# Performance work log

Hardware: AMD Instinct MI355X
Metric: run time of the kernel (lower is better)

## Reference

```python
import jax, jax.numpy as jnp
import numpy as np

B, S, D_IN, D = 2, 192, 1024, 128  # batch, seq_len, input_dim, triaffine_dim


def setup_inputs() -> dict:
    key = jax.random.key(0)
    ks = jax.random.split(key, 10)
    g = lambda k, sh, sc: jax.random.normal(k, sh, jnp.float32) * sc
    return {
        "x": g(ks[0], (B, S, D_IN), 1.0),
        "Wp": g(ks[1], (D_IN, D), 0.02), "bp": jnp.zeros((D,), jnp.float32),
        "Wh": g(ks[2], (D_IN, D), 0.02), "bh": jnp.zeros((D,), jnp.float32),
        "Wt": g(ks[3], (D_IN, D), 0.02), "bt": jnp.zeros((D,), jnp.float32),
        "W_span_ph": g(ks[4], (D, D, D), 0.02),
        "W_span_pt": g(ks[5], (D, D, D), 0.02),
        "W_ph_sib": g(ks[6], (D, D, D), 0.02),
        "W_pt_sib": g(ks[7], (D, D, D), 0.02),
        "W_ph_cop": g(ks[8], (D, D, D), 0.02),
        "W_pt_cop": g(ks[9], (D, D, D), 0.02),
    }


def _mlp(x, W, b):
    # supar-style MLP: Linear + LeakyReLU(0.1); dropout is identity at eval time
    return jax.nn.leaky_relu(x @ W + b, negative_slope=0.1)


def _triaffine(x, y, z, w):
    # supar Triaffine (n_out=1, no bias): s[b,z,x,y] = x_i W_ikj z_k y_j
    wz = jnp.einsum('bzk,ikj->bzij', z, w)          # [b,s,d,d]
    return jnp.einsum('bxi,bzij,byj->bzxy', x, wz, y)  # [b,s,s,s]


def _sym(s):
    # s.triu() + s.triu(1).transpose(-1,-2) over last two dims
    n = s.shape[-1]
    up = jnp.triu(jnp.ones((n, n), bool))
    up1 = jnp.triu(jnp.ones((n, n), bool), 1)
    zero = jnp.zeros((), s.dtype)
    return jnp.where(up, s, zero) + jnp.swapaxes(jnp.where(up1, s, zero), -1, -2)


def reference(x, Wp, bp, Wh, bh, Wt, bt,
              W_span_ph, W_span_pt, W_ph_sib, W_pt_sib, W_ph_cop, W_pt_cop):
    p = _mlp(x, Wp, bp)
    sh = _mlp(x, Wh, bh)   # shared_span: sh_mlp = h_mlp
    st = _mlp(x, Wt, bt)   # shared_span: st_mlp = t_mlp
    span_pst = _sym(_triaffine(sh, st, p, W_span_pt))
    span_psh = _sym(_triaffine(sh, st, p, W_span_ph))
    ph_sib = _sym(_triaffine(sh, sh, p, W_ph_sib))
    pt_sib = _sym(_triaffine(st, st, p, W_pt_sib))
    # co-parent scores: [b,z,x,y] -> permute(0,2,3,1) -> [b,x,y,z]
    ph_cop = jnp.transpose(_triaffine(p, p, sh, W_ph_cop), (0, 2, 3, 1))
    pt_cop = jnp.transpose(_sym(_triaffine(p, p, st, W_pt_cop)), (0, 2, 3, 1))
    return (span_psh, span_pst, ph_sib, pt_sib, ph_cop, pt_cop)
```

## Files before the change

### kernel.cpp

```cpp
#include <hip/hip_runtime.h>

#define SS 192
#define DD 128
#define SAN 16384
#define PITCH 136

typedef short bf8v __attribute__((ext_vector_type(8)));
typedef float f4v  __attribute__((ext_vector_type(4)));

__device__ __forceinline__ unsigned short f2bf(float f) {
    union { float f; unsigned u; } v; v.f = f;
    unsigned r = v.u + 0x7fffu + ((v.u >> 16) & 1u);
    return (unsigned short)(r >> 16);
}

__device__ __forceinline__ f4v mfma16(bf8v a, bf8v b, f4v c) {
    return __builtin_amdgcn_mfma_f32_16x16x32_bf16(a, b, c, 0, 0, 0);
}

__global__ __launch_bounds__(256) void proj_part(
    const float* __restrict__ x,
    const float* __restrict__ Wp, const float* __restrict__ Wh,
    const float* __restrict__ Wt, float* __restrict__ part)
{
    __shared__ float xs[8 * 256];
    int r0 = blockIdx.x * 8;
    int w  = blockIdx.y;
    int kc = blockIdx.z;
    const float* W = (w == 0) ? Wp : (w == 1) ? Wh : Wt;
    int tid = threadIdx.x;
    for (int u = tid; u < 512; u += 256) {
        int row = u >> 6, k4 = u & 63;
        *(float4*)(&xs[row * 256 + k4 * 4]) =
            *(const float4*)(&x[(size_t)(r0 + row) * 1024 + kc * 256 + k4 * 4]);
    }
    __syncthreads();
    int col = tid & 127, rg = tid >> 7;
    float acc[4] = {0.f, 0.f, 0.f, 0.f};
    const float* Wk = W + (size_t)(kc * 256) * 128 + col;
    #pragma unroll 8
    for (int k = 0; k < 256; ++k) {
        float wv = Wk[(size_t)k * 128];
        #pragma unroll
        for (int r = 0; r < 4; ++r) acc[r] += xs[(rg * 4 + r) * 256 + k] * wv;
    }
    float* pp = part + (((size_t)w * 4 + kc) * 384) * 128;
    #pragma unroll
    for (int r = 0; r < 4; ++r)
        pp[(size_t)(r0 + rg * 4 + r) * 128 + col] = acc[r];
}

__global__ __launch_bounds__(256) void proj_fin(
    const float* __restrict__ part,
    const float* __restrict__ bp, const float* __restrict__ bh,
    const float* __restrict__ bt,
    unsigned short* __restrict__ Pb, unsigned short* __restrict__ SHb,
    unsigned short* __restrict__ STb)
{
    int r0 = blockIdx.x * 8;
    int w  = blockIdx.y;
    const float* bias = (w == 0) ? bp : (w == 1) ? bh : bt;
    unsigned short* O = (w == 0) ? Pb : (w == 1) ? SHb : STb;
    int tid = threadIdx.x;
    int col = tid & 127, rg = tid >> 7;
    const float* pw = part + ((size_t)w * 4) * 384 * 128;
    float bb = bias[col];
    #pragma unroll
    for (int r = 0; r < 4; ++r) {
        int row = r0 + rg * 4 + r;
        float s = pw[(size_t)row * 128 + col]
                + pw[(size_t)(384 + row) * 128 + col]
                + pw[(size_t)(2 * 384 + row) * 128 + col]
                + pw[(size_t)(3 * 384 + row) * 128 + col];
        s += bb;
        s = s > 0.f ? s : 0.1f * s;
        O[(size_t)row * 128 + col] = f2bf(s);
    }
}

__global__ __launch_bounds__(256) void prep_rev(
    const float* __restrict__ w0, const float* __restrict__ w1,
    const float* __restrict__ w2, const float* __restrict__ w3,
    unsigned short* __restrict__ Wprep)
{
    __shared__ float tile[32][33];
    int sel = blockIdx.z;
    const float* in = (sel == 0) ? w0 : (sel == 1) ? w1 : (sel == 2) ? w2 : w3;
    unsigned short* out = Wprep + (size_t)sel * 2097152;
    int i  = blockIdx.y;
    int kt = (blockIdx.x >> 2) * 32, jt = (blockIdx.x & 3) * 32;
    int tx = threadIdx.x & 31, ty = threadIdx.x >> 5;
    #pragma unroll
    for (int r = 0; r < 4; ++r) {
        int k = kt + ty + r * 8;
        tile[ty + r * 8][tx] = in[((size_t)i * 128 + k) * 128 + jt + tx];
    }
    __syncthreads();
    #pragma unroll
    for (int r = 0; r < 4; ++r) {
        int j = jt + ty + r * 8;
        out[((size_t)j * 128 + i) * 128 + kt + tx] = f2bf(tile[tx][ty + r * 8]);
    }
}

__global__ __launch_bounds__(256) void prep_cop(
    const float* __restrict__ in0, const float* __restrict__ in1,
    unsigned short* __restrict__ Wprep)
{
    __shared__ float tile[32][33];
    int sel = blockIdx.z;
    const float* in = sel ? in1 : in0;
    unsigned short* out = Wprep + (size_t)(4 + sel) * 2097152;
    int k  = blockIdx.y;
    int it = (blockIdx.x >> 2) * 32, jt = (blockIdx.x & 3) * 32;
    int tx = threadIdx.x & 31, ty = threadIdx.x >> 5;
    #pragma unroll
    for (int r = 0; r < 4; ++r) {
        int i = it + ty + r * 8;
        tile[ty + r * 8][tx] = in[((size_t)i * 128 + k) * 128 + jt + tx];
    }
    __syncthreads();
    #pragma unroll
    for (int r = 0; r < 4; ++r) {
        int j = jt + ty + r * 8;
        out[((size_t)j * 128 + k) * 128 + it + tx] = f2bf(tile[tx][ty + r * 8]);
    }
}

__global__ __launch_bounds__(256) void stageA(
    const unsigned short* __restrict__ Pb,
    const unsigned short* __restrict__ Wprep, unsigned short* __restrict__ SAout)
{
    __shared__ unsigned short BL[64 * PITCH];
    int slot = blockIdx.y;
    int n0 = blockIdx.x * 64;
    const unsigned short* Wn = Wprep + (size_t)slot * 2097152 + (size_t)n0 * 128;
    unsigned short* Oo = SAout + (size_t)slot * ((size_t)384 * SAN);
    int tid = threadIdx.x;
    for (int u = tid; u < 1024; u += 256) {
        int e = u * 8; int r = e >> 7; int c = e & 127;
        *(uint4*)(&BL[r * PITCH + c]) = *(const uint4*)(&Wn[e]);
    }
    __syncthreads();
    int wave = tid >> 6, lane = tid & 63, m = lane & 15, quad = lane >> 4;
    const unsigned short* br = &BL[(wave * 16 + m) * PITCH + quad * 8];
    bf8v b0 = *(const bf8v*)(br);
    bf8v b1 = *(const bf8v*)(br + 32);
    bf8v b2 = *(const bf8v*)(br + 64);
    bf8v b3 = *(const bf8v*)(br + 96);
    for (int mt = 0; mt < 24; mt += 2) {
        const unsigned short* ar0 = Pb + (size_t)(mt * 16 + m) * 128 + quad * 8;
        const unsigned short* ar1 = ar0 + 16 * 128;
        f4v acc0 = {0.f, 0.f, 0.f, 0.f}, acc1 = {0.f, 0.f, 0.f, 0.f};
        acc0 = mfma16(*(const bf8v*)(ar0),      b0, acc0);
        acc1 = mfma16(*(const bf8v*)(ar1),      b0, acc1);
        acc0 = mfma16(*(const bf8v*)(ar0 + 32), b1, acc0);
        acc1 = mfma16(*(const bf8v*)(ar1 + 32), b1, acc1);
        acc0 = mfma16(*(const bf8v*)(ar0 + 64), b2, acc0);
        acc1 = mfma16(*(const bf8v*)(ar1 + 64), b2, acc1);
        acc0 = mfma16(*(const bf8v*)(ar0 + 96), b3, acc0);
        acc1 = mfma16(*(const bf8v*)(ar1 + 96), b3, acc1);
        unsigned short* orow0 = Oo + (size_t)(mt * 16) * SAN + n0 + wave * 16;
        unsigned short* orow1 = orow0 + (size_t)16 * SAN;
        #pragma unroll
        for (int r = 0; r < 4; ++r) {
            orow0[(size_t)(quad * 4 + r) * SAN + m] = f2bf(acc0[r]);
            orow1[(size_t)(quad * 4 + r) * SAN + m] = f2bf(acc1[r]);
        }
    }
}

__global__ __launch_bounds__(256, 3) void stageB_all(
    const unsigned short* __restrict__ Pb, const unsigned short* __restrict__ SHb,
    const unsigned short* __restrict__ STb, const unsigned short* __restrict__ SA,
    float* __restrict__ out)
{
    __shared__ unsigned short WZT[128 * PITCH];
    __shared__ unsigned short Tst[64 * PITCH];
    const size_t OUTN = (size_t)2 * SS * SS * SS;

    int t  = blockIdx.y;
    int bz = blockIdx.x;
    int b  = bz / SS;
    int tid = threadIdx.x;

    const unsigned short* src = SA + ((size_t)t * 384 + bz) * SAN;
    for (int u = tid; u < 2048; u += 256) {
        int e = u * 8; int j = e >> 7; int i = e & 127;
        *(uint4*)(&WZT[j * PITCH + i]) = *(const uint4*)(&src[e]);
    }
    __syncthreads();

    int wave = tid >> 6, lane = tid & 63, m = lane & 15, quad = lane >> 4;
    unsigned short* Trow = &Tst[wave * 16 * PITCH];
    const unsigned short* Ta = &Tst[(wave * 16 + m) * PITCH + quad * 8];

    if (t < 4) {
        const unsigned short* X = (t == 3) ? STb : SHb;
        const unsigned short* Y = (t == 2) ? SHb : STb;
        float* O = out + (size_t)t * OUTN + (size_t)bz * SS * SS;
        const unsigned short* Xb = X + (size_t)b * SS * DD;
        const unsigned short* Yb = Y + (size_t)b * SS * DD;

        int mts[3];
        mts[0] = wave;
        mts[1] = 7 - wave;
        mts[2] = (wave < 2) ? 9 - wave : 8 + wave;

        bf8v ta[3][4];
        #pragma unroll
        for (int mi = 0; mi < 3; ++mi) {
            int mt = mts[mi];
            const unsigned short* xr = Xb + (size_t)(mt * 16 + m) * DD + quad * 8;
            bf8v a0 = *(const bf8v*)(xr);
            bf8v a1 = *(const bf8v*)(xr + 32);
            bf8v a2 = *(const bf8v*)(xr + 64);
            bf8v a3 = *(const bf8v*)(xr + 96);
            for (int nt = 0; nt < 8; nt += 2) {
                f4v acc0 = {0.f,0.f,0.f,0.f}, acc1 = {0.f,0.f,0.f,0.f};
                const unsigned short* w0 = &WZT[(nt * 16 + m) * PITCH + quad * 8];
                const unsigned short* w1 = &WZT[((nt + 1) * 16 + m) * PITCH + quad * 8];
                acc0 = mfma16(a0, *(const bf8v*)(w0),      acc0);
                acc1 = mfma16(a0, *(const bf8v*)(w1),      acc1);
                acc0 = mfma16(a1, *(const bf8v*)(w0 + 32), acc0);
                acc1 = mfma16(a1, *(const bf8v*)(w1 + 32), acc1);
                acc0 = mfma16(a2, *(const bf8v*)(w0 + 64), acc0);
                acc1 = mfma16(a2, *(const bf8v*)(w1 + 64), acc1);
                acc0 = mfma16(a3, *(const bf8v*)(w0 + 96), acc0);
                acc1 = mfma16(a3, *(const bf8v*)(w1 + 96), acc1);
                #pragma unroll
                for (int r = 0; r < 4; ++r) {
                    Trow[(quad * 4 + r) * PITCH + nt * 16 + m]       = f2bf(acc0[r]);
                    Trow[(quad * 4 + r) * PITCH + (nt + 1) * 16 + m] = f2bf(acc1[r]);
                }
            }
            ta[mi][0] = *(const bf8v*)(Ta);
            ta[mi][1] = *(const bf8v*)(Ta + 32);
            ta[mi][2] = *(const bf8v*)(Ta + 64);
            ta[mi][3] = *(const bf8v*)(Ta + 96);
        }

        for (int yt = mts[0]; yt < 12; ++yt) {
            const unsigned short* yr = Yb + (size_t)(yt * 16 + m) * DD + quad * 8;
            bf8v yv0 = *(const bf8v*)(yr);
            bf8v yv1 = *(const bf8v*)(yr + 32);
            bf8v yv2 = *(const bf8v*)(yr + 64);
            bf8v yv3 = *(const bf8v*)(yr + 96);
            f4v accs[3];
            #pragma unroll
            for (int mi = 0; mi < 3; ++mi) {
                f4v acc = {0.f,0.f,0.f,0.f};
                acc = mfma16(ta[mi][0], yv0, acc);
                acc = mfma16(ta[mi][1], yv1, acc);
                acc = mfma16(ta[mi][2], yv2, acc);
                acc = mfma16(ta[mi][3], yv3, acc);
                accs[mi] = acc;
            }
            #pragma unroll
            for (int mi = 0; mi < 3; ++mi) {
                int mt = mts[mi];
                if (mt > yt) continue;
                f4v acc = accs[mi];
                int xs_ = mt * 16, ys_ = yt * 16, cc = m;
                if (mt == yt) {
                    #pragma unroll
                    for (int r = 0; r < 4; ++r) {
                        int rr = quad * 4 + r;
                        if (rr <= cc) O[(size_t)(xs_ + rr) * SS + xs_ + cc] = acc[r];
                        if (cc > rr)  O[(size_t)(xs_ + cc) * SS + xs_ + rr] = acc[r];
                    }
                } else {
                    #pragma unroll
                    for (int r = 0; r < 4; ++r)
                        O[(size_t)(xs_ + quad * 4 + r) * SS + ys_ + cc] = acc[r];
                    *(f4v*)(&O[(size_t)(ys_ + cc) * SS + xs_ + quad * 4]) = acc;
                }
            }
        }
    } else {
        const unsigned short* Zsrc = (t == 4) ? SHb : STb;
        int x  = bz - b * SS;
        int xt = x >> 4;
        float* Od = out + (size_t)t * OUTN + (size_t)bz * SS * SS;
        float* Om = out + (size_t)t * OUTN + (size_t)b * SS * SS * SS;

        bf8v tb[3][4];
        #pragma unroll
        for (int zi = 0; zi < 3; ++zi) {
            int zt = wave * 3 + zi;
            const unsigned short* sr = Zsrc + (size_t)(b * SS + zt * 16 + m) * DD + quad * 8;
            bf8v a0 = *(const bf8v*)(sr);
            bf8v a1 = *(const bf8v*)(sr + 32);
            bf8v a2 = *(const bf8v*)(sr + 64);
            bf8v a3 = *(const bf8v*)(sr + 96);
            for (int jt = 0; jt < 8; jt += 2) {
                f4v acc0 = {0.f,0.f,0.f,0.f}, acc1 = {0.f,0.f,0.f,0.f};
                const unsigned short* w0 = &WZT[(jt * 16 + m) * PITCH + quad * 8];
                const unsigned short* w1 = &WZT[((jt + 1) * 16 + m) * PITCH + quad * 8];
                acc0 = mfma16(a0, *(const bf8v*)(w0),      acc0);
                acc1 = mfma16(a0, *(const bf8v*)(w1),      acc1);
                acc0 = mfma16(a1, *(const bf8v*)(w0 + 32), acc0);
                acc1 = mfma16(a1, *(const bf8v*)(w1 + 32), acc1);
                acc0 = mfma16(a2, *(const bf8v*)(w0 + 64), acc0);
                acc1 = mfma16(a2, *(const bf8v*)(w1 + 64), acc1);
                acc0 = mfma16(a3, *(const bf8v*)(w0 + 96), acc0);
                acc1 = mfma16(a3, *(const bf8v*)(w1 + 96), acc1);
                #pragma unroll
                for (int r = 0; r < 4; ++r) {
                    Trow[(quad * 4 + r) * PITCH + jt * 16 + m]       = f2bf(acc0[r]);
                    Trow[(quad * 4 + r) * PITCH + (jt + 1) * 16 + m] = f2bf(acc1[r]);
                }
            }
            tb[zi][0] = *(const bf8v*)(Ta);
            tb[zi][1] = *(const bf8v*)(Ta + 32);
            tb[zi][2] = *(const bf8v*)(Ta + 64);
            tb[zi][3] = *(const bf8v*)(Ta + 96);
        }

        const unsigned short* Pbase = Pb + (size_t)b * SS * DD;
        int yt0 = (t == 4) ? 0 : xt;
        for (int yt = yt0; yt < 12; ++yt) {
            const unsigned short* pr = Pbase + (size_t)(yt * 16 + m) * DD + quad * 8;
            bf8v pv0 = *(const bf8v*)(pr);
            bf8v pv1 = *(const bf8v*)(pr + 32);
            bf8v pv2 = *(const bf8v*)(pr + 64);
            bf8v pv3 = *(const bf8v*)(pr + 96);
            f4v accs[3];
            #pragma unroll
            for (int zi = 0; zi < 3; ++zi) {
                f4v acc = {0.f,0.f,0.f,0.f};
                acc = mfma16(pv0, tb[zi][0], acc);
                acc = mfma16(pv1, tb[zi][1], acc);
                acc = mfma16(pv2, tb[zi][2], acc);
                acc = mfma16(pv3, tb[zi][3], acc);
                accs[zi] = acc;
            }
            if (t == 4) {
                #pragma unroll
                for (int zi = 0; zi < 3; ++zi) {
                    int zc = (wave * 3 + zi) * 16 + m;
                    #pragma unroll
                    for (int r = 0; r < 4; ++r)
                        Od[(size_t)(yt * 16 + quad * 4 + r) * SS + zc] = accs[zi][r];
                }
            } else if (yt == xt) {
                #pragma unroll
                for (int zi = 0; zi < 3; ++zi) {
                    int zc = (wave * 3 + zi) * 16 + m;
                    #pragma unroll
                    for (int r = 0; r < 4; ++r) {
                        int y = yt * 16 + quad * 4 + r;
                        if (y >= x) Od[(size_t)y * SS + zc] = accs[zi][r];
                        if (y > x)  Om[(size_t)y * SS * SS + (size_t)x * SS + zc] = accs[zi][r];
                    }
                }
            } else {
                #pragma unroll
                for (int zi = 0; zi < 3; ++zi) {
                    int zc = (wave * 3 + zi) * 16 + m;
                    #pragma unroll
                    for (int r = 0; r < 4; ++r) {
                        int y = yt * 16 + quad * 4 + r;
                        Od[(size_t)y * SS + zc] = accs[zi][r];
                        Om[(size_t)y * SS * SS + (size_t)x * SS + zc] = accs[zi][r];
                    }
                }
            }
        }
    }
}

extern "C" void kernel_launch(void* const* d_in, const int* in_sizes, int n_in,
                              void* d_out, int out_size, void* d_ws, size_t ws_size,
                              hipStream_t stream)
{
    const float* x   = (const float*)d_in[0];
    const float* Wp  = (const float*)d_in[1];
    const float* bp  = (const float*)d_in[2];
    const float* Wh  = (const float*)d_in[3];
    const float* bh  = (const float*)d_in[4];
    const float* Wt  = (const float*)d_in[5];
    const float* bt  = (const float*)d_in[6];
    const float* W_span_ph = (const float*)d_in[7];
    const float* W_span_pt = (const float*)d_in[8];
    const float* W_ph_sib  = (const float*)d_in[9];
    const float* W_pt_sib  = (const float*)d_in[10];
    const float* W_ph_cop  = (const float*)d_in[11];
    const float* W_pt_cop  = (const float*)d_in[12];

    char* ws = (char*)d_ws;
    unsigned short* Pb    = (unsigned short*)ws;
    unsigned short* SHb   = Pb + 384 * 128;
    unsigned short* STb   = SHb + 384 * 128;
    unsigned short* Wprep = (unsigned short*)(ws + 294912);
    unsigned short* SA    = (unsigned short*)(ws + 294912 + (size_t)6 * 2097152 * 2);
    float* part = (float*)SA;

    float* out  = (float*)d_out;

    proj_part<<<dim3(48, 3, 4), 256, 0, stream>>>(x, Wp, Wh, Wt, part);
    proj_fin<<<dim3(48, 3), 256, 0, stream>>>(part, bp, bh, bt, Pb, SHb, STb);
    prep_rev<<<dim3(16, 128, 4), 256, 0, stream>>>(W_span_ph, W_span_pt, W_ph_sib,
                                                   W_pt_sib, Wprep);
    prep_cop<<<dim3(16, 128, 2), 256, 0, stream>>>(W_ph_cop, W_pt_cop, Wprep);
    stageA<<<dim3(256, 6), 256, 0, stream>>>(Pb, Wprep, SA);
    stageB_all<<<dim3(384, 6), 256, 0, stream>>>(Pb, SHb, STb, SA, out);
}
```

Before: 563.6 us.

## Double stageB block to 8 waves, rebalance tiles, pack bf16 LDS stores, merge prep kernels

StageB now launches 512 threads (8 waves) per block instead of 4, and each wave handles one or two 16-row tiles instead of three. The symmetric span paths pair tiles wave and 15-wave so the triangular work stays balanced. Phase-1 results are computed with swapped MFMA operands so each lane writes packed bf16 pairs to LDS with one 64-bit store instead of scalar 16-bit scatter stores. The two weight-prep kernels are merged into one launch. The larger Tst buffer doubles LDS per block and may cut occupancy, and the new pairing leaves some waves with uneven work.

```diff
diff --git a/kernel.cpp b/kernel.cpp
--- a/kernel.cpp
+++ b/kernel.cpp
@@ -12,6 +12,10 @@
     union { float f; unsigned u; } v; v.f = f;
     unsigned r = v.u + 0x7fffu + ((v.u >> 16) & 1u);
     return (unsigned short)(r >> 16);
+}
+
+__device__ __forceinline__ unsigned pack2(float a, float b) {
+    return (unsigned)f2bf(a) | ((unsigned)f2bf(b) << 16);
 }
 
 __device__ __forceinline__ f4v mfma16(bf8v a, bf8v b, f4v c) {
@@ -78,52 +82,34 @@
     }
 }
 
-__global__ __launch_bounds__(256) void prep_rev(
+__global__ __launch_bounds__(256) void prep_all(
     const float* __restrict__ w0, const float* __restrict__ w1,
     const float* __restrict__ w2, const float* __restrict__ w3,
+    const float* __restrict__ w4, const float* __restrict__ w5,
     unsigned short* __restrict__ Wprep)
 {
     __shared__ float tile[32][33];
     int sel = blockIdx.z;
-    const float* in = (sel == 0) ? w0 : (sel == 1) ? w1 : (sel == 2) ? w2 : w3;
+    const float* in = (sel == 0) ? w0 : (sel == 1) ? w1 : (sel == 2) ? w2
+                    : (sel == 3) ? w3 : (sel == 4) ? w4 : w5;
     unsigned short* out = Wprep + (size_t)sel * 2097152;
-    int i  = blockIdx.y;
-    int kt = (blockIdx.x >> 2) * 32, jt = (blockIdx.x & 3) * 32;
+    int a  = blockIdx.y;
+    int ct = (blockIdx.x >> 2) * 32, jt = (blockIdx.x & 3) * 32;
     int tx = threadIdx.x & 31, ty = threadIdx.x >> 5;
-    #pragma unroll
-    for (int r = 0; r < 4; ++r) {
-        int k = kt + ty + r * 8;
-        tile[ty + r * 8][tx] = in[((size_t)i * 128 + k) * 128 + jt + tx];
+    if (sel < 4) {
+        #pragma unroll
+        for (int r = 0; r < 4; ++r)
+            tile[ty + r * 8][tx] = in[((size_t)a * 128 + ct + ty + r * 8) * 128 + jt + tx];
+    } else {
+        #pragma unroll
+        for (int r = 0; r < 4; ++r)
+            tile[ty + r * 8][tx] = in[((size_t)(ct + ty + r * 8) * 128 + a) * 128 + jt + tx];
     }
     __syncthreads();
     #pragma unroll
     for (int r = 0; r < 4; ++r) {
         int j = jt + ty + r * 8;
-        out[((size_t)j * 128 + i) * 128 + kt + tx] = f2bf(tile[tx][ty + r * 8]);
-    }
-}
-
-__global__ __launch_bounds__(256) void prep_cop(
-    const float* __restrict__ in0, const float* __restrict__ in1,
-    unsigned short* __restrict__ Wprep)
-{
-    __shared__ float tile[32][33];
-    int sel = blockIdx.z;
-    const float* in = sel ? in1 : in0;
-    unsigned short* out = Wprep + (size_t)(4 + sel) * 2097152;
-    int k  = blockIdx.y;
-    int it = (blockIdx.x >> 2) * 32, jt = (blockIdx.x & 3) * 32;
-    int tx = threadIdx.x & 31, ty = threadIdx.x >> 5;
-    #pragma unroll
-    for (int r = 0; r < 4; ++r) {
-        int i = it + ty + r * 8;
-        tile[ty + r * 8][tx] = in[((size_t)i * 128 + k) * 128 + jt + tx];
-    }
-    __syncthreads();
-    #pragma unroll
-    for (int r = 0; r < 4; ++r) {
-        int j = jt + ty + r * 8;
-        out[((size_t)j * 128 + k) * 128 + it + tx] = f2bf(tile[tx][ty + r * 8]);
+        out[((size_t)j * 128 + a) * 128 + ct + tx] = f2bf(tile[tx][ty + r * 8]);
     }
 }
 
@@ -170,13 +156,13 @@
     }
 }
 
-__global__ __launch_bounds__(256, 3) void stageB_all(
+__global__ __launch_bounds__(512, 4) void stageB_all(
     const unsigned short* __restrict__ Pb, const unsigned short* __restrict__ SHb,
     const unsigned short* __restrict__ STb, const unsigned short* __restrict__ SA,
     float* __restrict__ out)
 {
     __shared__ unsigned short WZT[128 * PITCH];
-    __shared__ unsigned short Tst[64 * PITCH];
+    __shared__ unsigned short Tst[128 * PITCH];
     const size_t OUTN = (size_t)2 * SS * SS * SS;
 
     int t  = blockIdx.y;
@@ -185,15 +171,45 @@
     int tid = threadIdx.x;
 
     const unsigned short* src = SA + ((size_t)t * 384 + bz) * SAN;
-    for (int u = tid; u < 2048; u += 256) {
+    for (int u = tid; u < 2048; u += 512) {
         int e = u * 8; int j = e >> 7; int i = e & 127;
         *(uint4*)(&WZT[j * PITCH + i]) = *(const uint4*)(&src[e]);
     }
     __syncthreads();
 
     int wave = tid >> 6, lane = tid & 63, m = lane & 15, quad = lane >> 4;
-    unsigned short* Trow = &Tst[wave * 16 * PITCH];
-    const unsigned short* Ta = &Tst[(wave * 16 + m) * PITCH + quad * 8];
+    unsigned short* TrowB = &Tst[(size_t)wave * 16 * PITCH];
+    const unsigned short* Ta = &Tst[((size_t)wave * 16 + m) * PITCH + quad * 8];
+
+    auto phase1 = [&](const unsigned short* fr, bf8v* tout) {
+        bf8v a0 = *(const bf8v*)(fr);
+        bf8v a1 = *(const bf8v*)(fr + 32);
+        bf8v a2 = *(const bf8v*)(fr + 64);
+        bf8v a3 = *(const bf8v*)(fr + 96);
+        #pragma unroll
+        for (int jt = 0; jt < 8; jt += 2) {
+            const unsigned short* w0 = &WZT[(jt * 16 + m) * PITCH + quad * 8];
+            const unsigned short* w1 = w0 + 16 * PITCH;
+            f4v acc0 = {0.f,0.f,0.f,0.f}, acc1 = {0.f,0.f,0.f,0.f};
+            acc0 = mfma16(*(const bf8v*)(w0),      a0, acc0);
+            acc1 = mfma16(*(const bf8v*)(w1),      a0, acc1);
+            acc0 = mfma16(*(const bf8v*)(w0 + 32), a1, acc0);
+            acc1 = mfma16(*(const bf8v*)(w1 + 32), a1, acc1);
+            acc0 = mfma16(*(const bf8v*)(w0 + 64), a2, acc0);
+            acc1 = mfma16(*(const bf8v*)(w1 + 64), a2, acc1);
+            acc0 = mfma16(*(const bf8v*)(w0 + 96), a3, acc0);
+            acc1 = mfma16(*(const bf8v*)(w1 + 96), a3, acc1);
+            uint2 v0, v1;
+            v0.x = pack2(acc0[0], acc0[1]); v0.y = pack2(acc0[2], acc0[3]);
+            v1.x = pack2(acc1[0], acc1[1]); v1.y = pack2(acc1[2], acc1[3]);
+            *(uint2*)(&TrowB[m * PITCH + jt * 16 + quad * 4])       = v0;
+            *(uint2*)(&TrowB[m * PITCH + (jt + 1) * 16 + quad * 4]) = v1;
+        }
+        tout[0] = *(const bf8v*)(Ta);
+        tout[1] = *(const bf8v*)(Ta + 32);
+        tout[2] = *(const bf8v*)(Ta + 64);
+        tout[3] = *(const bf8v*)(Ta + 96);
+    };
 
     if (t < 4) {
         const unsigned short* X = (t == 3) ? STb : SHb;
@@ -202,78 +218,62 @@
         const unsigned short* Xb = X + (size_t)b * SS * DD;
         const unsigned short* Yb = Y + (size_t)b * SS * DD;
 
-        int mts[3];
-        mts[0] = wave;
-        mts[1] = 7 - wave;
-        mts[2] = (wave < 2) ? 9 - wave : 8 + wave;
-
-        bf8v ta[3][4];
-        #pragma unroll
-        for (int mi = 0; mi < 3; ++mi) {
-            int mt = mts[mi];
-            const unsigned short* xr = Xb + (size_t)(mt * 16 + m) * DD + quad * 8;
-            bf8v a0 = *(const bf8v*)(xr);
-            bf8v a1 = *(const bf8v*)(xr + 32);
-            bf8v a2 = *(const bf8v*)(xr + 64);
-            bf8v a3 = *(const bf8v*)(xr + 96);
-            for (int nt = 0; nt < 8; nt += 2) {
-                f4v acc0 = {0.f,0.f,0.f,0.f}, acc1 = {0.f,0.f,0.f,0.f};
-                const unsigned short* w0 = &WZT[(nt * 16 + m) * PITCH + quad * 8];
-                const unsigned short* w1 = &WZT[((nt + 1) * 16 + m) * PITCH + quad * 8];
-                acc0 = mfma16(a0, *(const bf8v*)(w0),      acc0);
-                acc1 = mfma16(a0, *(const bf8v*)(w1),      acc1);
-                acc0 = mfma16(a1, *(const bf8v*)(w0 + 32), acc0);
-                acc1 = mfma16(a1, *(const bf8v*)(w1 + 32), acc1);
-                acc0 = mfma16(a2, *(const bf8v*)(w0 + 64), acc0);
-                acc1 = mfma16(a2, *(const bf8v*)(w1 + 64), acc1);
-                acc0 = mfma16(a3, *(const bf8v*)(w0 + 96), acc0);
-                acc1 = mfma16(a3, *(const bf8v*)(w1 + 96), acc1);
-                #pragma unroll
-                for (int r = 0; r < 4; ++r) {
-                    Trow[(quad * 4 + r) * PITCH + nt * 16 + m]       = f2bf(acc0[r]);
-                    Trow[(quad * 4 + r) * PITCH + (nt + 1) * 16 + m] = f2bf(acc1[r]);
-                }
-            }
-            ta[mi][0] = *(const bf8v*)(Ta);
-            ta[mi][1] = *(const bf8v*)(Ta + 32);
-            ta[mi][2] = *(const bf8v*)(Ta + 64);
-            ta[mi][3] = *(const bf8v*)(Ta + 96);
-        }
-
-        for (int yt = mts[0]; yt < 12; ++yt) {
+        int mt0 = wave;
+        int mt1 = 15 - wave;
+        bool two = (wave >= 4);
+
+        bf8v ta0[4], ta1[4];
+        phase1(Xb + (size_t)(mt0 * 16 + m) * DD + quad * 8, ta0);
+        if (two) phase1(Xb + (size_t)(mt1 * 16 + m) * DD + quad * 8, ta1);
+
+        for (int yt = mt0; yt < 12; ++yt) {
             const unsigned short* yr = Yb + (size_t)(yt * 16 + m) * DD + quad * 8;
             bf8v yv0 = *(const bf8v*)(yr);
             bf8v yv1 = *(const bf8v*)(yr + 32);
             bf8v yv2 = *(const bf8v*)(yr + 64);
             bf8v yv3 = *(const bf8v*)(yr + 96);
-            f4v accs[3];
-            #pragma unroll
-            for (int mi = 0; mi < 3; ++mi) {
-                f4v acc = {0.f,0.f,0.f,0.f};
-                acc = mfma16(ta[mi][0], yv0, acc);
-                acc = mfma16(ta[mi][1], yv1, acc);
-                acc = mfma16(ta[mi][2], yv2, acc);
-                acc = mfma16(ta[mi][3], yv3, acc);
-                accs[mi] = acc;
-            }
-            #pragma unroll
-            for (int mi = 0; mi < 3; ++mi) {
-                int mt = mts[mi];
-                if (mt > yt) continue;
-                f4v acc = accs[mi];
-                int xs_ = mt * 16, ys_ = yt * 16, cc = m;
-                if (mt == yt) {
+            bool c1 = two && (yt >= mt1);
+            f4v acc0 = {0.f,0.f,0.f,0.f}, acc1 = {0.f,0.f,0.f,0.f};
+            acc0 = mfma16(ta0[0], yv0, acc0);
+            acc0 = mfma16(ta0[1], yv1, acc0);
+            acc0 = mfma16(ta0[2], yv2, acc0);
+            acc0 = mfma16(ta0[3], yv3, acc0);
+            if (c1) {
+                acc1 = mfma16(ta1[0], yv0, acc1);
+                acc1 = mfma16(ta1[1], yv1, acc1);
+                acc1 = mfma16(ta1[2], yv2, acc1);
+                acc1 = mfma16(ta1[3], yv3, acc1);
+            }
+            {
+                int xs_ = mt0 * 16, ys_ = yt * 16, cc = m;
+                if (yt == mt0) {
                     #pragma unroll
                     for (int r = 0; r < 4; ++r) {
                         int rr = quad * 4 + r;
-                        if (rr <= cc) O[(size_t)(xs_ + rr) * SS + xs_ + cc] = acc[r];
-                        if (cc > rr)  O[(size_t)(xs_ + cc) * SS + xs_ + rr] = acc[r];
+                        if (rr <= cc) O[(size_t)(xs_ + rr) * SS + xs_ + cc] = acc0[r];
+                        if (cc > rr)  O[(size_t)(xs_ + cc) * SS + xs_ + rr] = acc0[r];
                     }
                 } else {
                     #pragma unroll
                     for (int r = 0; r < 4; ++r)
-                        O[(size_t)(xs_ + quad * 4 + r) * SS + ys_ + cc] = acc[r];
-                    *(f4v*)(&O[(size_t)(ys_ + cc) * SS + xs_ + quad * 4]) = acc;
+                        O[(size_t)(xs_ + quad * 4 + r) * SS + ys_ + cc] = acc0[r];
+                    *(f4v*)(&O[(size_t)(ys_ + cc) * SS + xs_ + quad * 4]) = acc0;
+                }
+            }
+            if (c1) {
+                int xs_ = mt1 * 16, ys_ = yt * 16, cc = m;
+                if (yt == mt1) {
+                    #pragma unroll
+                    for (int r = 0; r < 4; ++r) {
+                        int rr = quad * 4 + r;
+                        if (rr <= cc) O[(size_t)(xs_ + rr) * SS + xs_ + cc] = acc1[r];
+                        if (cc > rr)  O[(size_t)(xs_ + cc) * SS + xs_ + rr] = acc1[r];
+                    }
+                } else {
+                    #pragma unroll
+                    for (int r = 0; r < 4; ++r)
+                        O[(size_t)(xs_ + quad * 4 + r) * SS + ys_ + cc] = acc1[r];
+                    *(f4v*)(&O[(size_t)(ys_ + cc) * SS + xs_ + quad * 4]) = acc1;
                 }
             }
         }
@@ -284,85 +284,72 @@
         float* Od = out + (size_t)t * OUTN + (size_t)bz * SS * SS;
         float* Om = out + (size_t)t * OUTN + (size_t)b * SS * SS * SS;
 
-        bf8v tb[3][4];
-        #pragma unroll
-        for (int zi = 0; zi < 3; ++zi) {
-            int zt = wave * 3 + zi;
-            const unsigned short* sr = Zsrc + (size_t)(b * SS + zt * 16 + m) * DD + quad * 8;
-            bf8v a0 = *(const bf8v*)(sr);
-            bf8v a1 = *(const bf8v*)(sr + 32);
-            bf8v a2 = *(const bf8v*)(sr + 64);
-            bf8v a3 = *(const bf8v*)(sr + 96);
-            for (int jt = 0; jt < 8; jt += 2) {
-                f4v acc0 = {0.f,0.f,0.f,0.f}, acc1 = {0.f,0.f,0.f,0.f};
-                const unsigned short* w0 = &WZT[(jt * 16 + m) * PITCH + quad * 8];
-                const unsigned short* w1 = &WZT[((jt + 1) * 16 + m) * PITCH + quad * 8];
-                acc0 = mfma16(a0, *(const bf8v*)(w0),      acc0);
-                acc1 = mfma16(a0, *(const bf8v*)(w1),      acc1);
-                acc0 = mfma16(a1, *(const bf8v*)(w0 + 32), acc0);
-                acc1 = mfma16(a1, *(const bf8v*)(w1 + 32), acc1);
-                acc0 = mfma16(a2, *(const bf8v*)(w0 + 64), acc0);
-                acc1 = mfma16(a2, *(const bf8v*)(w1 + 64), acc1);
-                acc0 = mfma16(a3, *(const bf8v*)(w0 + 96), acc0);
-                acc1 = mfma16(a3, *(const bf8v*)(w1 + 96), acc1);
-                #pragma unroll
-                for (int r = 0; r < 4; ++r) {
-                    Trow[(quad * 4 + r) * PITCH + jt * 16 + m]       = f2bf(acc0[r]);
-                    Trow[(quad * 4 + r) * PITCH + (jt + 1) * 16 + m] = f2bf(acc1[r]);
-                }
-            }
-            tb[zi][0] = *(const bf8v*)(Ta);
-            tb[zi][1] = *(const bf8v*)(Ta + 32);
-            tb[zi][2] = *(const bf8v*)(Ta + 64);
-            tb[zi][3] = *(const bf8v*)(Ta + 96);
-        }
+        int zt0 = wave;
+        int zt1 = wave + 8;
+        bool two = (wave < 4);
+
+        bf8v tb0[4], tb1[4];
+        phase1(Zsrc + (size_t)(b * SS + zt0 * 16 + m) * DD + quad * 8, tb0);
+        if (two) phase1(Zsrc + (size_t)(b * SS + zt1 * 16 + m) * DD + quad * 8, tb1);
 
         const unsigned short* Pbase = Pb + (size_t)b * SS * DD;
         int yt0 = (t == 4) ? 0 : xt;
+        int zc0 = zt0 * 16 + m, zc1 = zt1 * 16 + m;
+
         for (int yt = yt0; yt < 12; ++yt) {
             const unsigned short* pr = Pbase + (size_t)(yt * 16 + m) * DD + quad * 8;
             bf8v pv0 = *(const bf8v*)(pr);
             bf8v pv1 = *(const bf8v*)(pr + 32);
             bf8v pv2 = *(const bf8v*)(pr + 64);
             bf8v pv3 = *(const bf8v*)(pr + 96);
-            f4v accs[3];
-            #pragma unroll
-            for (int zi = 0; zi < 3; ++zi) {
-                f4v acc = {0.f,0.f,0.f,0.f};
-                acc = mfma16(pv0, tb[zi][0], acc);
-                acc = mfma16(pv1, tb[zi][1], acc);
-                acc = mfma16(pv2, tb[zi][2], acc);
-                acc = mfma16(pv3, tb[zi][3], acc);
-                accs[zi] = acc;
+            f4v acc0 = {0.f,0.f,0.f,0.f}, acc1 = {0.f,0.f,0.f,0.f};
+            acc0 = mfma16(pv0, tb0[0], acc0);
+            acc0 = mfma16(pv1, tb0[1], acc0);
+            acc0 = mfma16(pv2, tb0[2], acc0);
+            acc0 = mfma16(pv3, tb0[3], acc0);
+            if (two) {
+                acc1 = mfma16(pv0, tb1[0], acc1);
+                acc1 = mfma16(pv1, tb1[1], acc1);
+                acc1 = mfma16(pv2, tb1[2], acc1);
+                acc1 = mfma16(pv3, tb1[3], acc1);
             }
             if (t == 4) {
                 #pragma unroll
-                for (int zi = 0; zi < 3; ++zi) {
-                    int zc = (wave * 3 + zi) * 16 + m;
+                for (int r = 0; r < 4; ++r)
+                    Od[(size_t)(yt * 16 + quad * 4 + r) * SS + zc0] = acc0[r];
+                if (two) {
                     #pragma unroll
                     for (int r = 0; r < 4; ++r)
-                        Od[(size_t)(yt * 16 + quad * 4 + r) * SS + zc] = accs[zi][r];
+                        Od[(size_t)(yt * 16 + quad * 4 + r) * SS + zc1] = acc1[r];
                 }
             } else if (yt == xt) {
                 #pragma unroll
-                for (int zi = 0; zi < 3; ++zi) {
-                    int zc = (wave * 3 + zi) * 16 + m;
+                for (int r = 0; r < 4; ++r) {
+                    int y = yt * 16 + quad * 4 + r;
+                    if (y >= x) Od[(size_t)y * SS + zc0] = acc0[r];
+                    if (y > x)  Om[(size_t)y * SS * SS + (size_t)x * SS + zc0] = acc0[r];
+                }
+                if (two) {
                     #pragma unroll
                     for (int r = 0; r < 4; ++r) {
                         int y = yt * 16 + quad * 4 + r;
-                        if (y >= x) Od[(size_t)y * SS + zc] = accs[zi][r];
-                        if (y > x)  Om[(size_t)y * SS * SS + (size_t)x * SS + zc] = accs[zi][r];
+                        if (y >= x) Od[(size_t)y * SS + zc1] = acc1[r];
+                        if (y > x)  Om[(size_t)y * SS * SS + (size_t)x * SS + zc1] = acc1[r];
                     }
                 }
             } else {
                 #pragma unroll
-                for (int zi = 0; zi < 3; ++zi) {
-                    int zc = (wave * 3 + zi) * 16 + m;
+                for (int r = 0; r < 4; ++r) {
+                    int y = yt * 16 + quad * 4 + r;
+                    Od[(size_t)y * SS + zc0] = acc0[r];
+                    Om[(size_t)y * SS * SS + (size_t)x * SS + zc0] = acc0[r];
+                }
+                if (two) {
                     #pragma unroll
                     for (int r = 0; r < 4; ++r) {
                         int y = yt * 16 + quad * 4 + r;
-                        Od[(size_t)y * SS + zc] = accs[zi][r];
-                        Om[(size_t)y * SS * SS + (size_t)x * SS + zc] = accs[zi][r];
+                        Od[(size_t)y * SS + zc1] = acc1[r];
+                        Om[(size_t)y * SS * SS + (size_t)x * SS + zc1] = acc1[r];
                     }
                 }
             }
@@ -400,9 +387,8 @@
 
     proj_part<<<dim3(48, 3, 4), 256, 0, stream>>>(x, Wp, Wh, Wt, part);
     proj_fin<<<dim3(48, 3), 256, 0, stream>>>(part, bp, bh, bt, Pb, SHb, STb);
-    prep_rev<<<dim3(16, 128, 4), 256, 0, stream>>>(W_span_ph, W_span_pt, W_ph_sib,
-                                                   W_pt_sib, Wprep);
-    prep_cop<<<dim3(16, 128, 2), 256, 0, stream>>>(W_ph_cop, W_pt_cop, Wprep);
+    prep_all<<<dim3(16, 128, 6), 256, 0, stream>>>(W_span_ph, W_span_pt, W_ph_sib,
+                                                   W_pt_sib, W_ph_cop, W_pt_cop, Wprep);
     stageA<<<dim3(256, 6), 256, 0, stream>>>(Pb, Wprep, SA);
-    stageB_all<<<dim3(384, 6), 256, 0, stream>>>(Pb, SHb, STb, SA, out);
-}
+    stageB_all<<<dim3(384, 6), 512, 0, stream>>>(Pb, SHb, STb, SA, out);
+}
```

After: 624.1 us. 1.11x slower.
